# Kernel optimization log

Hardware: AMD Instinct MI355X
Metric: run time of the kernel (lower is better)

## Reference

```python
import jax, jax.numpy as jnp
import numpy as np

T, B, E = 2048, 2, 256
H = 8
D = E // H


def setup_inputs() -> dict:
    key = jax.random.key(0)
    ks = jax.random.split(key, 10)
    s = 1.0 / np.sqrt(E)
    return {
        "query": jax.random.normal(ks[0], (T, B, E), jnp.float32),
        "attn_bias": jax.random.normal(ks[1], (B, T, T), jnp.float32),
        "Wq": jax.random.normal(ks[2], (E, E), jnp.float32) * s,
        "bq": jax.random.normal(ks[3], (E,), jnp.float32) * 0.02,
        "Wk": jax.random.normal(ks[4], (E, E), jnp.float32) * s,
        "bk": jax.random.normal(ks[5], (E,), jnp.float32) * 0.02,
        "Wv": jax.random.normal(ks[6], (E, E), jnp.float32) * s,
        "bv": jax.random.normal(ks[7], (E,), jnp.float32) * 0.02,
        "Wo": jax.random.normal(ks[8], (E, E), jnp.float32) * s,
        "bo": jax.random.normal(ks[9], (E,), jnp.float32) * 0.02,
    }


def reference(query, attn_bias, Wq, bq, Wk, bk, Wv, bv, Wo, bo):
    # query: [T, B, E] (seq-first). Self-attention: k,v also projected from query.
    t, b, e = query.shape
    scaling = 1.0 / np.sqrt(D)
    q = (query @ Wq.T + bq) * scaling          # [T,B,E]
    k = query @ Wk.T + bk                      # [T,B,E]
    v = query @ Wv.T + bv                      # [T,B,E]
    q = q.reshape(t, b, H, D)
    k = k.reshape(t, b, H, D)
    v = v.reshape(t, b, H, D)
    # raw scores + per-batch additive bias broadcast across heads
    scores = jnp.einsum("tbhd,sbhd->bhts", q, k) + attn_bias[:, None, :, :]
    attn_weights = jax.nn.softmax(scores, axis=-1)  # [B,H,T,S]
    attn = jnp.einsum("bhts,sbhd->tbhd", attn_weights, v).reshape(t, b, e)
    return attn @ Wo.T + bo  # [T,B,E]
```

## Files before the change

### kernel.cpp

```cpp
#include <hip/hip_runtime.h>
#include <hip/hip_bf16.h>

#define T_DIM 2048
#define B_DIM 2
#define E_DIM 256
#define H_DIM 8
#define D_DIM 32
#define M_DIM (T_DIM*B_DIM)
#define SPLIT 4
#define S_CHUNK (T_DIM/SPLIT)

typedef __bf16 bf16x8 __attribute__((ext_vector_type(8)));
typedef __bf16 bf16x4 __attribute__((ext_vector_type(4)));
typedef float  f32x4  __attribute__((ext_vector_type(4)));

__global__ __launch_bounds__(256)
void qkv_kernel(const float* __restrict__ X,
                const float* __restrict__ Wq, const float* __restrict__ Wk, const float* __restrict__ Wv,
                const float* __restrict__ bq, const float* __restrict__ bk, const float* __restrict__ bv,
                __bf16* __restrict__ qh, __bf16* __restrict__ kperm, __bf16* __restrict__ vperm) {
    __shared__ __align__(16) __bf16 Xs[64][136];
    __shared__ __align__(16) __bf16 Ws[64][136];
    const int m0 = blockIdx.x * 64;
    const int which = blockIdx.y >> 2;
    const int n0 = (blockIdx.y & 3) * 64;
    const float* W = (which == 0) ? Wq : (which == 1) ? Wk : Wv;
    const float* bias = (which == 0) ? bq : (which == 1) ? bk : bv;
    const int tid = threadIdx.x;
    const int wid = tid >> 6, lane = tid & 63;
    const int wm = (wid & 1) * 32, wn = (wid >> 1) * 32;
    const int lr = lane & 15, lg = lane >> 4;

    f32x4 acc[2][2] = {};
    for (int kc = 0; kc < 2; ++kc) {
        for (int c = tid; c < 2048; c += 256) {
            int row = c >> 5, col = (c & 31) * 4;
            float4 xv = *(const float4*)&X[(size_t)(m0 + row) * E_DIM + kc * 128 + col];
            float4 wv = *(const float4*)&W[(size_t)(n0 + row) * E_DIM + kc * 128 + col];
            bf16x4 xb, wb;
            xb[0] = (__bf16)xv.x; xb[1] = (__bf16)xv.y; xb[2] = (__bf16)xv.z; xb[3] = (__bf16)xv.w;
            wb[0] = (__bf16)wv.x; wb[1] = (__bf16)wv.y; wb[2] = (__bf16)wv.z; wb[3] = (__bf16)wv.w;
            *(bf16x4*)&Xs[row][col] = xb;
            *(bf16x4*)&Ws[row][col] = wb;
        }
        __syncthreads();
#pragma unroll
        for (int ks = 0; ks < 4; ++ks) {
            bf16x8 a0 = *(const bf16x8*)&Xs[wm + lr][ks * 32 + lg * 8];
            bf16x8 a1 = *(const bf16x8*)&Xs[wm + 16 + lr][ks * 32 + lg * 8];
            bf16x8 b0 = *(const bf16x8*)&Ws[wn + lr][ks * 32 + lg * 8];
            bf16x8 b1 = *(const bf16x8*)&Ws[wn + 16 + lr][ks * 32 + lg * 8];
            acc[0][0] = __builtin_amdgcn_mfma_f32_16x16x32_bf16(a0, b0, acc[0][0], 0, 0, 0);
            acc[0][1] = __builtin_amdgcn_mfma_f32_16x16x32_bf16(a0, b1, acc[0][1], 0, 0, 0);
            acc[1][0] = __builtin_amdgcn_mfma_f32_16x16x32_bf16(a1, b0, acc[1][0], 0, 0, 0);
            acc[1][1] = __builtin_amdgcn_mfma_f32_16x16x32_bf16(a1, b1, acc[1][1], 0, 0, 0);
        }
        __syncthreads();
    }
    const float scale = 0.17677669529663687f;
#pragma unroll
    for (int mt = 0; mt < 2; ++mt) {
#pragma unroll
        for (int nt = 0; nt < 2; ++nt) {
            int n = n0 + wn + nt * 16 + lr;
            float bb = bias[n];
            int h = n >> 5, d = n & 31;
#pragma unroll
            for (int r = 0; r < 4; ++r) {
                int m = m0 + wm + mt * 16 + lg * 4 + r;
                int t = m >> 1, b = m & 1;
                float v = acc[mt][nt][r] + bb;
                if (which == 0) {
                    v *= scale;
                    qh[((size_t)(b * H_DIM + h) * T_DIM + t) * D_DIM + d] = (__bf16)v;
                } else if (which == 1) {
                    int til = t >> 6, s6 = t & 63;
                    int ntk = ((s6 >> 5) << 1) | ((s6 >> 2) & 1);
                    int lrk = (((s6 >> 3) & 3) << 2) | (s6 & 3);
                    int lanek = ((d >> 3) << 4) | lrk;
                    kperm[((((size_t)(b * H_DIM + h) * 32 + til) * 4 + ntk) * 64 + lanek) * 8 + (d & 7)] = (__bf16)v;
                } else {
                    int til = t >> 6;
                    int ktv = (t >> 5) & 1, lgv = (t >> 3) & 3, elv = t & 7;
                    int jv = ktv * 2 + (d >> 4);
                    int lanev = (lgv << 4) | (d & 15);
                    vperm[((((size_t)(b * H_DIM + h) * 32 + til) * 4 + jv) * 64 + lanev) * 8 + elv] = (__bf16)v;
                }
            }
        }
    }
}

__global__ __launch_bounds__(512, 4)
void attn_kernel(const __bf16* __restrict__ qh, const __bf16* __restrict__ kperm,
                 const __bf16* __restrict__ vperm, const float* __restrict__ attn_bias,
                 float* __restrict__ po, float* __restrict__ pl) {
    __shared__ __align__(16) float Bs[16][516];
    const int t0 = blockIdx.x * 16;
    const int b  = blockIdx.y;
    const int sp = blockIdx.z;
    const int tid = threadIdx.x, wid = tid >> 6, lane = tid & 63;
    const int lr = lane & 15, lg = lane >> 4;
    const int bh = b * H_DIM + wid;
    const int sbase = sp * S_CHUNK;
    const int tb0 = sp * (S_CHUNK / 64);
    const float LOG2E = 1.4426950408889634f;
    const float NM2 = -12.0f * LOG2E;

    {
        const float* bsrc = attn_bias + ((size_t)b * T_DIM + t0) * T_DIM + sbase;
        int r = tid >> 5, c0 = (tid & 31) * 4;
#pragma unroll
        for (int rep = 0; rep < 4; ++rep) {
            float4 v = *(const float4*)&bsrc[(size_t)r * T_DIM + rep * 128 + c0];
            *(float4*)&Bs[r][rep * 128 + c0] = v;
        }
    }
    __syncthreads();

    bf16x8 qf = *(const bf16x8*)&qh[((size_t)bh * T_DIM + t0 + lr) * D_DIM + lg * 8];
    const __bf16* kpb = kperm + (size_t)bh * T_DIM * D_DIM + (size_t)lane * 8;
    const __bf16* vpb = vperm + (size_t)bh * T_DIM * D_DIM + (size_t)lane * 8;

    f32x4 o0 = {}, o1 = {};
    f32x4 lacc = {};

#pragma unroll
    for (int st = 0; st < S_CHUNK / 64; ++st) {
        const int til = tb0 + st;

        bf16x8 kf0 = *(const bf16x8*)&kpb[(size_t)(til * 4 + 0) * 512];
        bf16x8 kf1 = *(const bf16x8*)&kpb[(size_t)(til * 4 + 1) * 512];
        bf16x8 kf2 = *(const bf16x8*)&kpb[(size_t)(til * 4 + 2) * 512];
        bf16x8 kf3 = *(const bf16x8*)&kpb[(size_t)(til * 4 + 3) * 512];
        bf16x8 vf0 = *(const bf16x8*)&vpb[(size_t)(til * 4 + 0) * 512];
        bf16x8 vf1 = *(const bf16x8*)&vpb[(size_t)(til * 4 + 1) * 512];
        bf16x8 vf2 = *(const bf16x8*)&vpb[(size_t)(til * 4 + 2) * 512];
        bf16x8 vf3 = *(const bf16x8*)&vpb[(size_t)(til * 4 + 3) * 512];

        f32x4 cb0 = *(const f32x4*)&Bs[lr][st * 64 +  0 + lg * 8 + 0];
        f32x4 cb1 = *(const f32x4*)&Bs[lr][st * 64 +  0 + lg * 8 + 4];
        f32x4 cb2 = *(const f32x4*)&Bs[lr][st * 64 + 32 + lg * 8 + 0];
        f32x4 cb3 = *(const f32x4*)&Bs[lr][st * 64 + 32 + lg * 8 + 4];

        f32x4 sv0 = __builtin_amdgcn_mfma_f32_16x16x32_bf16(kf0, qf, cb0, 0, 0, 0);
        f32x4 sv1 = __builtin_amdgcn_mfma_f32_16x16x32_bf16(kf1, qf, cb1, 0, 0, 0);
        f32x4 sv2 = __builtin_amdgcn_mfma_f32_16x16x32_bf16(kf2, qf, cb2, 0, 0, 0);
        f32x4 sv3 = __builtin_amdgcn_mfma_f32_16x16x32_bf16(kf3, qf, cb3, 0, 0, 0);

        f32x4 e0, e1, e2, e3;
#pragma unroll
        for (int r = 0; r < 4; ++r) {
            e0[r] = exp2f(fmaf(sv0[r], LOG2E, NM2));
            e1[r] = exp2f(fmaf(sv1[r], LOG2E, NM2));
            e2[r] = exp2f(fmaf(sv2[r], LOG2E, NM2));
            e3[r] = exp2f(fmaf(sv3[r], LOG2E, NM2));
        }
        lacc += e0; lacc += e1; lacc += e2; lacc += e3;

        bf16x8 pf0, pf1;
#pragma unroll
        for (int r = 0; r < 4; ++r) {
            pf0[r] = (__bf16)e0[r]; pf0[4 + r] = (__bf16)e1[r];
            pf1[r] = (__bf16)e2[r]; pf1[4 + r] = (__bf16)e3[r];
        }

        o0 = __builtin_amdgcn_mfma_f32_16x16x32_bf16(pf0, vf0, o0, 0, 0, 0);
        o1 = __builtin_amdgcn_mfma_f32_16x16x32_bf16(pf0, vf1, o1, 0, 0, 0);
        o0 = __builtin_amdgcn_mfma_f32_16x16x32_bf16(pf1, vf2, o0, 0, 0, 0);
        o1 = __builtin_amdgcn_mfma_f32_16x16x32_bf16(pf1, vf3, o1, 0, 0, 0);
    }

    float l = (lacc[0] + lacc[1]) + (lacc[2] + lacc[3]);
    l += __shfl_xor(l, 16);
    l += __shfl_xor(l, 32);

#pragma unroll
    for (int r = 0; r < 4; ++r) {
        int t = t0 + lg * 4 + r;
        size_t rw = ((size_t)bh * T_DIM + t) * SPLIT + sp;
        po[rw * D_DIM + lr]      = o0[r];
        po[rw * D_DIM + 16 + lr] = o1[r];
    }
    if (lg == 0)
        pl[((size_t)bh * T_DIM + t0 + lr) * SPLIT + sp] = l;
}

__global__ __launch_bounds__(256)
void combine_kernel(const float* __restrict__ po, const float* __restrict__ pl,
                    __bf16* __restrict__ attn) {
    int idx = blockIdx.x * 256 + threadIdx.x;
    int row = idx >> 3, dg = idx & 7;
    int bh = row >> 11, t = row & 2047;
    int b = bh >> 3, h = bh & 7;

    float L = 0.f;
    f32x4 acc = {};
#pragma unroll
    for (int s2 = 0; s2 < SPLIT; ++s2) {
        L += pl[(size_t)row * SPLIT + s2];
        f32x4 v = *(const f32x4*)&po[((size_t)row * SPLIT + s2) * D_DIM + dg * 4];
#pragma unroll
        for (int j = 0; j < 4; ++j) acc[j] += v[j];
    }
    float inv = 1.0f / L;
    bf16x4 o4;
#pragma unroll
    for (int j = 0; j < 4; ++j) o4[j] = (__bf16)(acc[j] * inv);
    *(bf16x4*)&attn[((size_t)(t * B_DIM + b)) * E_DIM + h * D_DIM + dg * 4] = o4;
}

__global__ __launch_bounds__(256)
void oproj_kernel(const __bf16* __restrict__ X, const float* __restrict__ Wo,
                  const float* __restrict__ bo, float* __restrict__ out) {
    __shared__ __align__(16) __bf16 Xs[64][136];
    __shared__ __align__(16) __bf16 Ws[64][136];
    const int m0 = blockIdx.x * 64;
    const int n0 = blockIdx.y * 64;
    const int tid = threadIdx.x;
    const int wid = tid >> 6, lane = tid & 63;
    const int wm = (wid & 1) * 32, wn = (wid >> 1) * 32;
    const int lr = lane & 15, lg = lane >> 4;

    f32x4 acc[2][2] = {};
    for (int kc = 0; kc < 2; ++kc) {
        for (int c = tid; c < 1024; c += 256) {
            int row = c >> 4, col = (c & 15) * 8;
            *(bf16x8*)&Xs[row][col] = *(const bf16x8*)&X[(size_t)(m0 + row) * E_DIM + kc * 128 + col];
        }
        for (int c = tid; c < 2048; c += 256) {
            int row = c >> 5, col = (c & 31) * 4;
            float4 wv = *(const float4*)&Wo[(size_t)(n0 + row) * E_DIM + kc * 128 + col];
            bf16x4 wb;
            wb[0] = (__bf16)wv.x; wb[1] = (__bf16)wv.y; wb[2] = (__bf16)wv.z; wb[3] = (__bf16)wv.w;
            *(bf16x4*)&Ws[row][col] = wb;
        }
        __syncthreads();
#pragma unroll
        for (int ks = 0; ks < 4; ++ks) {
            bf16x8 a0 = *(const bf16x8*)&Xs[wm + lr][ks * 32 + lg * 8];
            bf16x8 a1 = *(const bf16x8*)&Xs[wm + 16 + lr][ks * 32 + lg * 8];
            bf16x8 b0 = *(const bf16x8*)&Ws[wn + lr][ks * 32 + lg * 8];
            bf16x8 b1 = *(const bf16x8*)&Ws[wn + 16 + lr][ks * 32 + lg * 8];
            acc[0][0] = __builtin_amdgcn_mfma_f32_16x16x32_bf16(a0, b0, acc[0][0], 0, 0, 0);
            acc[0][1] = __builtin_amdgcn_mfma_f32_16x16x32_bf16(a0, b1, acc[0][1], 0, 0, 0);
            acc[1][0] = __builtin_amdgcn_mfma_f32_16x16x32_bf16(a1, b0, acc[1][0], 0, 0, 0);
            acc[1][1] = __builtin_amdgcn_mfma_f32_16x16x32_bf16(a1, b1, acc[1][1], 0, 0, 0);
        }
        __syncthreads();
    }
#pragma unroll
    for (int mt = 0; mt < 2; ++mt) {
#pragma unroll
        for (int nt = 0; nt < 2; ++nt) {
            int n = n0 + wn + nt * 16 + lr;
            float bb = bo[n];
#pragma unroll
            for (int r = 0; r < 4; ++r) {
                int m = m0 + wm + mt * 16 + lg * 4 + r;
                out[(size_t)m * E_DIM + n] = acc[mt][nt][r] + bb;
            }
        }
    }
}

extern "C" void kernel_launch(void* const* d_in, const int* in_sizes, int n_in,
                              void* d_out, int out_size, void* d_ws, size_t ws_size,
                              hipStream_t stream) {
    const float* query     = (const float*)d_in[0];
    const float* attn_bias = (const float*)d_in[1];
    const float* Wq = (const float*)d_in[2];
    const float* bq = (const float*)d_in[3];
    const float* Wk = (const float*)d_in[4];
    const float* bk = (const float*)d_in[5];
    const float* Wv = (const float*)d_in[6];
    const float* bv = (const float*)d_in[7];
    const float* Wo = (const float*)d_in[8];
    const float* bo = (const float*)d_in[9];
    float* out = (float*)d_out;

    char* ws = (char*)d_ws;
    __bf16* qhp  = (__bf16*)(ws);
    __bf16* kpp  = (__bf16*)(ws + 2097152);
    __bf16* vpp  = (__bf16*)(ws + 4194304);
    __bf16* attn = (__bf16*)(ws + 6291456);
    float*  po   = (float*)(ws + 8388608);
    float*  pl   = (float*)(ws + 25165824);

    qkv_kernel<<<dim3(M_DIM / 64, 12), 256, 0, stream>>>(
        query, Wq, Wk, Wv, bq, bk, bv, qhp, kpp, vpp);

    attn_kernel<<<dim3(T_DIM / 16, B_DIM, SPLIT), 512, 0, stream>>>(
        qhp, kpp, vpp, attn_bias, po, pl);
    combine_kernel<<<dim3(B_DIM * H_DIM * T_DIM * 8 / 256), 256, 0, stream>>>(po, pl, attn);

    oproj_kernel<<<dim3(M_DIM / 64, E_DIM / 64), 256, 0, stream>>>(attn, Wo, bo, out);
}
```

Measured before the change: 58.01 us.

## Double-buffer K/V fragment loads with inline asm and explicit vmcnt waits

Replaces the compiler-scheduled K/V global loads in the attention inner loop with hand-issued global_load_dwordx4 into two register buffers (A/B). Each tile's loads are issued one tile ahead and fenced with s_waitcnt vmcnt and sched_barrier, so memory latency overlaps the MFMA and exp work of the current tile. This costs extra VGPRs for the second buffer, which could pressure occupancy under launch_bounds(512,4). Because the asm outputs do not depend on the waits, correctness relies on the explicit waitcnts and scheduling barriers.

```diff
diff --git a/kernel.cpp b/kernel.cpp
--- a/kernel.cpp
+++ b/kernel.cpp
@@ -91,6 +91,41 @@
     }
 }
 
+#define GLOAD(dst, p) asm volatile("global_load_dwordx4 %0, %1, off" : "=v"(dst) : "v"(p))
+#define WAITV8()  asm volatile("s_waitcnt vmcnt(8)" ::: "memory")
+#define WAITV0()  asm volatile("s_waitcnt vmcnt(0)" ::: "memory")
+#define SBAR()    __builtin_amdgcn_sched_barrier(0)
+
+#define ATTN_TILE(ST, K0, K1, K2, K3, V0, V1, V2, V3) do {                           \
+    f32x4 cb0 = *(const f32x4*)&Bs[lr][(ST) * 64 + lg * 8 + 0];                      \
+    f32x4 cb1 = *(const f32x4*)&Bs[lr][(ST) * 64 + lg * 8 + 4];                      \
+    f32x4 cb2 = *(const f32x4*)&Bs[lr][(ST) * 64 + 32 + lg * 8 + 0];                 \
+    f32x4 cb3 = *(const f32x4*)&Bs[lr][(ST) * 64 + 32 + lg * 8 + 4];                 \
+    f32x4 sv0 = __builtin_amdgcn_mfma_f32_16x16x32_bf16(K0, qf, cb0, 0, 0, 0);       \
+    f32x4 sv1 = __builtin_amdgcn_mfma_f32_16x16x32_bf16(K1, qf, cb1, 0, 0, 0);       \
+    f32x4 sv2 = __builtin_amdgcn_mfma_f32_16x16x32_bf16(K2, qf, cb2, 0, 0, 0);       \
+    f32x4 sv3 = __builtin_amdgcn_mfma_f32_16x16x32_bf16(K3, qf, cb3, 0, 0, 0);       \
+    f32x4 e0, e1, e2, e3;                                                            \
+    _Pragma("unroll")                                                                \
+    for (int r = 0; r < 4; ++r) {                                                    \
+        e0[r] = exp2f(fmaf(sv0[r], LOG2E, NM2));                                     \
+        e1[r] = exp2f(fmaf(sv1[r], LOG2E, NM2));                                     \
+        e2[r] = exp2f(fmaf(sv2[r], LOG2E, NM2));                                     \
+        e3[r] = exp2f(fmaf(sv3[r], LOG2E, NM2));                                     \
+    }                                                                                \
+    lacc += e0; lacc += e1; lacc += e2; lacc += e3;                                  \
+    bf16x8 pf0, pf1;                                                                 \
+    _Pragma("unroll")                                                                \
+    for (int r = 0; r < 4; ++r) {                                                    \
+        pf0[r] = (__bf16)e0[r]; pf0[4 + r] = (__bf16)e1[r];                          \
+        pf1[r] = (__bf16)e2[r]; pf1[4 + r] = (__bf16)e3[r];                          \
+    }                                                                                \
+    o0 = __builtin_amdgcn_mfma_f32_16x16x32_bf16(pf0, V0, o0, 0, 0, 0);              \
+    o1 = __builtin_amdgcn_mfma_f32_16x16x32_bf16(pf0, V1, o1, 0, 0, 0);              \
+    o0 = __builtin_amdgcn_mfma_f32_16x16x32_bf16(pf1, V2, o0, 0, 0, 0);              \
+    o1 = __builtin_amdgcn_mfma_f32_16x16x32_bf16(pf1, V3, o1, 0, 0, 0);              \
+} while (0)
+
 __global__ __launch_bounds__(512, 4)
 void attn_kernel(const __bf16* __restrict__ qh, const __bf16* __restrict__ kperm,
                  const __bf16* __restrict__ vperm, const float* __restrict__ attn_bias,
@@ -103,7 +138,7 @@
     const int lr = lane & 15, lg = lane >> 4;
     const int bh = b * H_DIM + wid;
     const int sbase = sp * S_CHUNK;
-    const int tb0 = sp * (S_CHUNK / 64);
+    const int tb0 = sp * 8;
     const float LOG2E = 1.4426950408889634f;
     const float NM2 = -12.0f * LOG2E;
 
@@ -125,50 +160,51 @@
     f32x4 o0 = {}, o1 = {};
     f32x4 lacc = {};
 
-#pragma unroll
-    for (int st = 0; st < S_CHUNK / 64; ++st) {
-        const int til = tb0 + st;
-
-        bf16x8 kf0 = *(const bf16x8*)&kpb[(size_t)(til * 4 + 0) * 512];
-        bf16x8 kf1 = *(const bf16x8*)&kpb[(size_t)(til * 4 + 1) * 512];
-        bf16x8 kf2 = *(const bf16x8*)&kpb[(size_t)(til * 4 + 2) * 512];
-        bf16x8 kf3 = *(const bf16x8*)&kpb[(size_t)(til * 4 + 3) * 512];
-        bf16x8 vf0 = *(const bf16x8*)&vpb[(size_t)(til * 4 + 0) * 512];
-        bf16x8 vf1 = *(const bf16x8*)&vpb[(size_t)(til * 4 + 1) * 512];
-        bf16x8 vf2 = *(const bf16x8*)&vpb[(size_t)(til * 4 + 2) * 512];
-        bf16x8 vf3 = *(const bf16x8*)&vpb[(size_t)(til * 4 + 3) * 512];
-
-        f32x4 cb0 = *(const f32x4*)&Bs[lr][st * 64 +  0 + lg * 8 + 0];
-        f32x4 cb1 = *(const f32x4*)&Bs[lr][st * 64 +  0 + lg * 8 + 4];
-        f32x4 cb2 = *(const f32x4*)&Bs[lr][st * 64 + 32 + lg * 8 + 0];
-        f32x4 cb3 = *(const f32x4*)&Bs[lr][st * 64 + 32 + lg * 8 + 4];
-
-        f32x4 sv0 = __builtin_amdgcn_mfma_f32_16x16x32_bf16(kf0, qf, cb0, 0, 0, 0);
-        f32x4 sv1 = __builtin_amdgcn_mfma_f32_16x16x32_bf16(kf1, qf, cb1, 0, 0, 0);
-        f32x4 sv2 = __builtin_amdgcn_mfma_f32_16x16x32_bf16(kf2, qf, cb2, 0, 0, 0);
-        f32x4 sv3 = __builtin_amdgcn_mfma_f32_16x16x32_bf16(kf3, qf, cb3, 0, 0, 0);
-
-        f32x4 e0, e1, e2, e3;
-#pragma unroll
-        for (int r = 0; r < 4; ++r) {
-            e0[r] = exp2f(fmaf(sv0[r], LOG2E, NM2));
-            e1[r] = exp2f(fmaf(sv1[r], LOG2E, NM2));
-            e2[r] = exp2f(fmaf(sv2[r], LOG2E, NM2));
-            e3[r] = exp2f(fmaf(sv3[r], LOG2E, NM2));
-        }
-        lacc += e0; lacc += e1; lacc += e2; lacc += e3;
-
-        bf16x8 pf0, pf1;
-#pragma unroll
-        for (int r = 0; r < 4; ++r) {
-            pf0[r] = (__bf16)e0[r]; pf0[4 + r] = (__bf16)e1[r];
-            pf1[r] = (__bf16)e2[r]; pf1[4 + r] = (__bf16)e3[r];
-        }
-
-        o0 = __builtin_amdgcn_mfma_f32_16x16x32_bf16(pf0, vf0, o0, 0, 0, 0);
-        o1 = __builtin_amdgcn_mfma_f32_16x16x32_bf16(pf0, vf1, o1, 0, 0, 0);
-        o0 = __builtin_amdgcn_mfma_f32_16x16x32_bf16(pf1, vf2, o0, 0, 0, 0);
-        o1 = __builtin_amdgcn_mfma_f32_16x16x32_bf16(pf1, vf3, o1, 0, 0, 0);
+    bf16x8 kA0, kA1, kA2, kA3, vA0, vA1, vA2, vA3;
+    bf16x8 kB0, kB1, kB2, kB3, vB0, vB1, vB2, vB3;
+
+    GLOAD(kA0, kpb + (size_t)(tb0 * 4 + 0) * 512);
+    GLOAD(kA1, kpb + (size_t)(tb0 * 4 + 1) * 512);
+    GLOAD(kA2, kpb + (size_t)(tb0 * 4 + 2) * 512);
+    GLOAD(kA3, kpb + (size_t)(tb0 * 4 + 3) * 512);
+    GLOAD(vA0, vpb + (size_t)(tb0 * 4 + 0) * 512);
+    GLOAD(vA1, vpb + (size_t)(tb0 * 4 + 1) * 512);
+    GLOAD(vA2, vpb + (size_t)(tb0 * 4 + 2) * 512);
+    GLOAD(vA3, vpb + (size_t)(tb0 * 4 + 3) * 512);
+
+#pragma unroll
+    for (int st = 0; st < 8; st += 2) {
+        {
+            const int tB = tb0 + st + 1;
+            GLOAD(kB0, kpb + (size_t)(tB * 4 + 0) * 512);
+            GLOAD(kB1, kpb + (size_t)(tB * 4 + 1) * 512);
+            GLOAD(kB2, kpb + (size_t)(tB * 4 + 2) * 512);
+            GLOAD(kB3, kpb + (size_t)(tB * 4 + 3) * 512);
+            GLOAD(vB0, vpb + (size_t)(tB * 4 + 0) * 512);
+            GLOAD(vB1, vpb + (size_t)(tB * 4 + 1) * 512);
+            GLOAD(vB2, vpb + (size_t)(tB * 4 + 2) * 512);
+            GLOAD(vB3, vpb + (size_t)(tB * 4 + 3) * 512);
+        }
+        WAITV8();
+        SBAR();
+        ATTN_TILE(st, kA0, kA1, kA2, kA3, vA0, vA1, vA2, vA3);
+
+        if (st + 2 < 8) {
+            const int tA = tb0 + st + 2;
+            GLOAD(kA0, kpb + (size_t)(tA * 4 + 0) * 512);
+            GLOAD(kA1, kpb + (size_t)(tA * 4 + 1) * 512);
+            GLOAD(kA2, kpb + (size_t)(tA * 4 + 2) * 512);
+            GLOAD(kA3, kpb + (size_t)(tA * 4 + 3) * 512);
+            GLOAD(vA0, vpb + (size_t)(tA * 4 + 0) * 512);
+            GLOAD(vA1, vpb + (size_t)(tA * 4 + 1) * 512);
+            GLOAD(vA2, vpb + (size_t)(tA * 4 + 2) * 512);
+            GLOAD(vA3, vpb + (size_t)(tA * 4 + 3) * 512);
+            WAITV8();
+        } else {
+            WAITV0();
+        }
+        SBAR();
+        ATTN_TILE(st + 1, kB0, kB1, kB2, kB3, vB0, vB1, vB2, vB3);
     }
 
     float l = (lacc[0] + lacc[1]) + (lacc[2] + lacc[3]);
```

New measurement: 59.84 us. 3.2% more time.
